# Performance work log

Measured on AMD Instinct MI355X. Metric: run time of the kernel, lower is better.

## Reference

```python
import jax, jax.numpy as jnp
import numpy as np

D_IN = 1024
D_OUT = 1024
NUM_HEADS = 16
HEAD_DIM = D_OUT // NUM_HEADS


def setup_inputs() -> dict:
    key = jax.random.key(0)
    ks = jax.random.split(key, 6)
    b, T = 2, 2048
    scale = 0.02
    x = jax.random.normal(ks[0], (b, T, D_IN), dtype=jnp.float32)
    Wq = jax.random.normal(ks[1], (D_IN, D_OUT), dtype=jnp.float32) * scale
    Wk = jax.random.normal(ks[2], (D_IN, D_OUT), dtype=jnp.float32) * scale
    Wv = jax.random.normal(ks[3], (D_IN, D_OUT), dtype=jnp.float32) * scale
    Wo = jax.random.normal(ks[4], (D_OUT, D_OUT), dtype=jnp.float32) * scale
    bo = jnp.zeros((D_OUT,), dtype=jnp.float32)
    return {"x": x, "Wq": Wq, "Wk": Wk, "Wv": Wv, "Wo": Wo, "bo": bo}


def reference(x, Wq, Wk, Wv, Wo, bo):
    b, T, _ = x.shape
    H, Dh = NUM_HEADS, HEAD_DIM
    # projections: [b,T,d_out] -> [b,H,T,Dh]
    q = (x @ Wq).reshape(b, T, H, Dh).transpose(0, 2, 1, 3)
    k = (x @ Wk).reshape(b, T, H, Dh).transpose(0, 2, 1, 3)
    v = (x @ Wv).reshape(b, T, H, Dh).transpose(0, 2, 1, 3)
    # scores: [b,H,T,T]
    att = jnp.einsum('bhqd,bhkd->bhqk', q, k)
    causal = jnp.triu(jnp.ones((T, T), dtype=bool), k=1)
    att = jnp.where(causal, -jnp.inf, att)
    att = jax.nn.softmax(att / np.sqrt(Dh).astype(np.float32), axis=-1)
    # dropout p=0.0 -> identity
    y = jnp.einsum('bhqk,bhkd->bhqd', att, v)
    y = y.transpose(0, 2, 1, 3).reshape(b, T, H * Dh)
    return y @ Wo + bo
```

## Files before the change

### kernel.cpp

```cpp
#include <hip/hip_runtime.h>

#define T_   2048
#define DM   1024
#define H_   16
#define DH   64

typedef unsigned short u16;
typedef unsigned int u32;
typedef __attribute__((ext_vector_type(8))) short bf16x8;
typedef __attribute__((ext_vector_type(8))) unsigned short u16x8;
typedef __attribute__((ext_vector_type(4))) float f32x4;
typedef __attribute__((ext_vector_type(16))) float f32x16;
typedef __attribute__((ext_vector_type(4))) unsigned int u32x4;
typedef __attribute__((ext_vector_type(2))) unsigned int u32x2;

static __device__ __forceinline__ u16 f2b(float f) {
  unsigned int u = __builtin_bit_cast(unsigned int, f);
  u += 0x7fff + ((u >> 16) & 1);
  return (u16)(u >> 16);
}

static __device__ __forceinline__ u32 cvtpk(float a, float b) {
  u32 d;
  asm("v_cvt_pk_bf16_f32 %0, %1, %2" : "=v"(d) : "v"(a), "v"(b));
  return d;
}

static __device__ __forceinline__ void gll16(const void* g, void* l) {
  __builtin_amdgcn_global_load_lds(
      (const __attribute__((address_space(1))) unsigned int*)g,
      (__attribute__((address_space(3))) unsigned int*)l, 16, 0, 0);
}

static __device__ __forceinline__ bf16x8 ldf(const char* base, int rho,
                                             int k16) {
  return *(const bf16x8*)(base + rho * 128 + ((k16 ^ (rho & 7)) << 4));
}


__global__ __launch_bounds__(256) void k_cvt_x(const float* __restrict__ x,
                                               u16* __restrict__ o) {
  int i = (blockIdx.x * 256 + threadIdx.x) * 8;
  float4 a = *(const float4*)(x + i);
  float4 b = *(const float4*)(x + i + 4);
  u16x8 r;
  r[0] = f2b(a.x); r[1] = f2b(a.y); r[2] = f2b(a.z); r[3] = f2b(a.w);
  r[4] = f2b(b.x); r[5] = f2b(b.y); r[6] = f2b(b.z); r[7] = f2b(b.w);
  *(u16x8*)(o + i) = r;
}

__global__ __launch_bounds__(256) void k_cvt_wt(
    const float* __restrict__ Wq, const float* __restrict__ Wk,
    const float* __restrict__ Wv, const float* __restrict__ Wo,
    u16* __restrict__ oq, u16* __restrict__ ok, u16* __restrict__ ov,
    u16* __restrict__ oo) {
  const float* W; u16* Wt;
  int z = blockIdx.z;
  if (z == 0)      { W = Wq; Wt = oq; }
  else if (z == 1) { W = Wk; Wt = ok; }
  else if (z == 2) { W = Wv; Wt = ov; }
  else             { W = Wo; Wt = oo; }
  const float wsc = (z == 0) ? 0.1803368801111204f : 1.0f;
  __shared__ u16 tile[64][65];
  int k0 = blockIdx.x * 64, n0 = blockIdx.y * 64;
  int r = threadIdx.x >> 2, c0 = (threadIdx.x & 3) * 16;
  const float* src = W + (k0 + r) * DM + n0 + c0;
#pragma unroll
  for (int e = 0; e < 16; e += 4) {
    float4 v = *(const float4*)(src + e);
    tile[r][c0 + e + 0] = f2b(v.x * wsc);
    tile[r][c0 + e + 1] = f2b(v.y * wsc);
    tile[r][c0 + e + 2] = f2b(v.z * wsc);
    tile[r][c0 + e + 3] = f2b(v.w * wsc);
  }
  __syncthreads();
  u16x8 a, b;
#pragma unroll
  for (int e = 0; e < 8; ++e) a[e] = tile[c0 + e][r];
#pragma unroll
  for (int e = 0; e < 8; ++e) b[e] = tile[c0 + 8 + e][r];
  u16* dst = Wt + (n0 + r) * DM + k0 + c0;
  *(u16x8*)dst = a;
  *(u16x8*)(dst + 8) = b;
}

__global__ __launch_bounds__(256) void k_qkv(
    const u16* __restrict__ X, const u16* __restrict__ Wqt,
    const u16* __restrict__ Wkt, const u16* __restrict__ Wvt,
    u16* __restrict__ Qg, u16* __restrict__ Kg, u16* __restrict__ Vtg) {
  __shared__ char smem[34816];
  char* As = smem;
  char* Bs = smem + 16384;
  const int tid = threadIdx.x, lane = tid & 63, w = tid >> 6;
  const int frow = lane & 15, fk = lane >> 4;
  const int wr = (w >> 1) * 64, wc = (w & 1) * 64;
  const int m0 = blockIdx.x * 128;
  const int by = blockIdx.y;
  const int z = by >> 3, n0 = (by & 7) * 128;
  const u16* Wt = (z == 0) ? Wqt : (z == 1) ? Wkt : Wvt;
  const u16* Ap = X + m0 * DM;
  const u16* Bp = Wt + n0 * DM;
  const int ro = lane >> 3;
  const int ce = ((lane & 7) ^ ro) << 3;

  f32x4 acc[4][4];
#pragma unroll
  for (int mi = 0; mi < 4; ++mi)
#pragma unroll
    for (int ni = 0; ni < 4; ++ni) acc[mi][ni] = (f32x4){0.f, 0.f, 0.f, 0.f};

  for (int k0 = 0; k0 < DM; k0 += 64) {
#pragma unroll
    for (int c = 0; c < 4; ++c) {
      const int g8 = (w * 4 + c) * 8;
      gll16(Ap + (g8 + ro) * DM + k0 + ce, As + g8 * 128);
      gll16(Bp + (g8 + ro) * DM + k0 + ce, Bs + g8 * 128);
    }
    asm volatile("s_waitcnt vmcnt(0)" ::: "memory");
    __syncthreads();
    bf16x8 a[4][2], b[4][2];
#pragma unroll
    for (int mi = 0; mi < 4; ++mi)
#pragma unroll
      for (int kk = 0; kk < 2; ++kk)
        a[mi][kk] = ldf(As, wr + mi * 16 + frow, kk * 4 + fk);
#pragma unroll
    for (int ni = 0; ni < 4; ++ni)
#pragma unroll
      for (int kk = 0; kk < 2; ++kk)
        b[ni][kk] = ldf(Bs, wc + ni * 16 + frow, kk * 4 + fk);
#pragma unroll
    for (int mi = 0; mi < 4; ++mi)
#pragma unroll
      for (int ni = 0; ni < 4; ++ni)
#pragma unroll
        for (int kk = 0; kk < 2; ++kk)
          acc[mi][ni] = __builtin_amdgcn_mfma_f32_16x16x32_bf16(
              a[mi][kk], b[ni][kk], acc[mi][ni], 0, 0, 0);
    __syncthreads();
  }

  if (z < 2) {
    u16* out = (z == 0) ? Qg : Kg;
#pragma unroll
    for (int mi = 0; mi < 4; ++mi)
#pragma unroll
      for (int ni = 0; ni < 4; ++ni)
#pragma unroll
        for (int r = 0; r < 4; ++r) {
          int m = m0 + wr + mi * 16 + fk * 4 + r;
          int nl = n0 + wc + ni * 16 + frow;
          int b = m >> 11, t = m & 2047, h = nl >> 6, d = nl & 63;
          out[((b * H_ + h) * T_ + t) * DH + d] = f2b(acc[mi][ni][r]);
        }
  } else {
    u16* Tl = (u16*)smem;
#pragma unroll
    for (int ni = 0; ni < 4; ++ni) {
      const int n = wc + ni * 16 + frow;
#pragma unroll
      for (int mi = 0; mi < 4; ++mi)
#pragma unroll
        for (int r = 0; r < 4; ++r)
          Tl[n * 136 + wr + mi * 16 + fk * 4 + r] = f2b(acc[mi][ni][r]);
    }
    __syncthreads();
    const int n = tid >> 1, c0 = (tid & 1) * 64;
    const int ng = n0 + n, h = ng >> 6, d = ng & 63;
    const int b = m0 >> 11;
    const int tb = (m0 & 2047) + c0;
    u16* dst = Vtg + ((b * H_ + h) * DH + d) * T_ + tb;
#pragma unroll
    for (int e = 0; e < 8; ++e)
      *(u16x8*)(dst + e * 8) = *(const u16x8*)(Tl + n * 136 + c0 + e * 8);
  }
}

__global__ __launch_bounds__(256) void k_out(
    const u16* __restrict__ Y, const u16* __restrict__ Wot,
    const float* __restrict__ bo, float* __restrict__ out) {
  __shared__ char smem[24576];
  char* As = smem;
  char* Bs = smem + 8192;
  const int tid = threadIdx.x, lane = tid & 63, w = tid >> 6;
  const int frow = lane & 15, fk = lane >> 4;
  const int wr = (w >> 1) * 32, wc = (w & 1) * 64;
  const int m0 = blockIdx.x * 64, n0 = blockIdx.y * 128;
  const u16* Ap = Y + m0 * DM;
  const u16* Bp = Wot + n0 * DM;
  const int ro = lane >> 3;
  const int ce = ((lane & 7) ^ ro) << 3;

  f32x4 acc[2][4];
#pragma unroll
  for (int mi = 0; mi < 2; ++mi)
#pragma unroll
    for (int ni = 0; ni < 4; ++ni) acc[mi][ni] = (f32x4){0.f, 0.f, 0.f, 0.f};

  for (int k0 = 0; k0 < DM; k0 += 64) {
#pragma unroll
    for (int c = 0; c < 2; ++c) {
      const int g8 = (w * 2 + c) * 8;
      gll16(Ap + (g8 + ro) * DM + k0 + ce, As + g8 * 128);
    }
#pragma unroll
    for (int c = 0; c < 4; ++c) {
      const int g8 = (w * 4 + c) * 8;
      gll16(Bp + (g8 + ro) * DM + k0 + ce, Bs + g8 * 128);
    }
    asm volatile("s_waitcnt vmcnt(0)" ::: "memory");
    __syncthreads();
    bf16x8 a[2][2], b[4][2];
#pragma unroll
    for (int mi = 0; mi < 2; ++mi)
#pragma unroll
      for (int kk = 0; kk < 2; ++kk)
        a[mi][kk] = ldf(As, wr + mi * 16 + frow, kk * 4 + fk);
#pragma unroll
    for (int ni = 0; ni < 4; ++ni)
#pragma unroll
      for (int kk = 0; kk < 2; ++kk)
        b[ni][kk] = ldf(Bs, wc + ni * 16 + frow, kk * 4 + fk);
#pragma unroll
    for (int mi = 0; mi < 2; ++mi)
#pragma unroll
      for (int ni = 0; ni < 4; ++ni)
#pragma unroll
        for (int kk = 0; kk < 2; ++kk)
          acc[mi][ni] = __builtin_amdgcn_mfma_f32_16x16x32_bf16(
              a[mi][kk], b[ni][kk], acc[mi][ni], 0, 0, 0);
    __syncthreads();
  }
#pragma unroll
  for (int mi = 0; mi < 2; ++mi)
#pragma unroll
    for (int ni = 0; ni < 4; ++ni)
#pragma unroll
      for (int r = 0; r < 4; ++r) {
        int m = m0 + wr + mi * 16 + fk * 4 + r;
        int n = n0 + wc + ni * 16 + frow;
        out[m * DM + n] = acc[mi][ni][r] + bo[n];
      }
}

__global__ __launch_bounds__(64) void k_attn(
    const u16* __restrict__ Qg, const u16* __restrict__ Kg,
    const u16* __restrict__ Vtg, u16* __restrict__ Yg) {
  __shared__ char Kl[8192];
  __shared__ char Vl[8192];
  const int bh = blockIdx.x;
  const int qt = 63 - blockIdx.y;
  const int q0 = qt * 32;
  const int lane = threadIdx.x;
  const int hi = lane >> 5, qq = lane & 31;
  const u16* Qb = Qg + bh * (T_ * DH);
  const u16* Kb = Kg + bh * (T_ * DH);
  const u16* Vb = Vtg + bh * (DH * T_);
  const int qrow = q0 + qq;

  bf16x8 qf[4];
#pragma unroll
  for (int kb = 0; kb < 4; ++kb)
    qf[kb] = *(const bf16x8*)(Qb + qrow * DH + kb * 16 + hi * 8);

  f32x16 o0, o1;
#pragma unroll
  for (int r = 0; r < 16; ++r) { o0[r] = 0.f; o1[r] = 0.f; }
  float m = -1e30f, lp = 0.f;

  const int nt = (qt >> 1) + 1;
  const int ro = lane >> 3;
  const int ce = ((lane & 7) ^ ro) << 3;

#pragma unroll
  for (int g = 0; g < 8; ++g)
    gll16(Kb + (g * 8 + ro) * DH + ce, Kl + g * 1024);
#pragma unroll
  for (int g = 0; g < 8; ++g)
    gll16(Vb + (g * 8 + ro) * T_ + ce, Vl + g * 1024);

  for (int t = 0; t < nt; ++t) {
    const bool st = (t + 1 < nt);
    const int jn = (t + 1) * 64;
    asm volatile("s_waitcnt vmcnt(8)" ::: "memory");
    bf16x8 kf[8];
#pragma unroll
    for (int kb = 0; kb < 4; ++kb) {
      kf[kb] = *(const bf16x8*)(
          Kl + qq * 128 + (((kb * 2 + hi) ^ (qq & 7)) << 4));
      kf[4 + kb] = *(const bf16x8*)(
          Kl + (qq + 32) * 128 + (((kb * 2 + hi) ^ (qq & 7)) << 4));
    }
    asm volatile("s_waitcnt lgkmcnt(0)" ::: "memory");
    if (st) {
#pragma unroll
      for (int g = 0; g < 8; ++g)
        gll16(Kb + (jn + g * 8 + ro) * DH + ce, Kl + g * 1024);
    }
    f32x16 s0, s1;
#pragma unroll
    for (int r = 0; r < 16; ++r) { s0[r] = 0.f; s1[r] = 0.f; }
#pragma unroll
    for (int kb = 0; kb < 4; ++kb) {
      s0 = __builtin_amdgcn_mfma_f32_32x32x16_bf16(kf[kb], qf[kb], s0, 0, 0, 0);
      s1 = __builtin_amdgcn_mfma_f32_32x32x16_bf16(kf[4 + kb], qf[kb], s1, 0, 0, 0);
    }
    if (t == nt - 1) {
      const int j0 = t * 64;
#pragma unroll
      for (int r = 0; r < 16; ++r) {
        const int cr = j0 + (r & 3) + 8 * (r >> 2) + 4 * hi;
        if (cr > qrow) s0[r] = -1e30f;
        if (cr + 32 > qrow) s1[r] = -1e30f;
      }
    }
    float tm[16];
#pragma unroll
    for (int r = 0; r < 16; ++r) tm[r] = fmaxf(s0[r], s1[r]);
#pragma unroll
    for (int stp = 8; stp > 0; stp >>= 1)
#pragma unroll
      for (int r = 0; r < stp; ++r) tm[r] = fmaxf(tm[r], tm[r + stp]);
    const float mt = fmaxf(tm[0], __shfl_xor(tm[0], 32));
    if (__any(mt > m + 8.f)) {
      const float mn = fmaxf(m, mt);
      const float al = __builtin_amdgcn_exp2f(m - mn);
      m = mn;
#pragma unroll
      for (int r = 0; r < 16; ++r) { o0[r] *= al; o1[r] *= al; }
      lp *= al;
    }
    float ts[16];
#pragma unroll
    for (int r = 0; r < 16; ++r) {
      s0[r] = __builtin_amdgcn_exp2f(s0[r] - m);
      s1[r] = __builtin_amdgcn_exp2f(s1[r] - m);
      ts[r] = s0[r] + s1[r];
    }
#pragma unroll
    for (int stp = 8; stp > 0; stp >>= 1)
#pragma unroll
      for (int r = 0; r < stp; ++r) ts[r] += ts[r + stp];
    lp += ts[0];
    bf16x8 pb[4];
#define MKCH(DST, S, RB)                                                     \
  {                                                                          \
    u32 a01 = cvtpk(S[RB + 0], S[RB + 1]);                                   \
    u32 a23 = cvtpk(S[RB + 2], S[RB + 3]);                                   \
    u32 a45 = cvtpk(S[RB + 4], S[RB + 5]);                                   \
    u32 a67 = cvtpk(S[RB + 6], S[RB + 7]);                                   \
    asm volatile("v_permlane32_swap_b32 %0, %1" : "+v"(a01), "+v"(a45));     \
    asm volatile("v_permlane32_swap_b32 %0, %1" : "+v"(a23), "+v"(a67));     \
    u32x4 t4;                                                                \
    t4[0] = a01; t4[1] = a23; t4[2] = a45; t4[3] = a67;                      \
    DST = __builtin_bit_cast(bf16x8, t4);                                    \
  }
    MKCH(pb[0], s0, 0)
    MKCH(pb[1], s0, 8)
    MKCH(pb[2], s1, 0)
    MKCH(pb[3], s1, 8)
#undef MKCH
    if (st) { asm volatile("s_waitcnt vmcnt(8)" ::: "memory"); }
    else    { asm volatile("s_waitcnt vmcnt(0)" ::: "memory"); }
    bf16x8 vf[8];
#pragma unroll
    for (int jc = 0; jc < 4; ++jc) {
      vf[jc] = *(const bf16x8*)(
          Vl + qq * 128 + (((jc * 2 + hi) ^ (qq & 7)) << 4));
      vf[4 + jc] = *(const bf16x8*)(
          Vl + (qq + 32) * 128 + (((jc * 2 + hi) ^ (qq & 7)) << 4));
    }
    asm volatile("s_waitcnt lgkmcnt(0)" ::: "memory");
    if (st) {
#pragma unroll
      for (int g = 0; g < 8; ++g)
        gll16(Vb + (g * 8 + ro) * T_ + jn + ce, Vl + g * 1024);
    }
#pragma unroll
    for (int jc = 0; jc < 4; ++jc) {
      o0 = __builtin_amdgcn_mfma_f32_32x32x16_bf16(vf[jc], pb[jc], o0, 0, 0, 0);
      o1 = __builtin_amdgcn_mfma_f32_32x32x16_bf16(vf[4 + jc], pb[jc], o1, 0, 0, 0);
    }
  }
  lp += __shfl_xor(lp, 32);
  const float rl = 1.0f / lp;
  const int obase = ((bh >> 4) * T_ + qrow) * DM + (bh & 15) * DH;
#pragma unroll
  for (int g = 0; g < 4; ++g) {
    u32x2 st;
    st[0] = cvtpk(o0[g * 4 + 0] * rl, o0[g * 4 + 1] * rl);
    st[1] = cvtpk(o0[g * 4 + 2] * rl, o0[g * 4 + 3] * rl);
    *(u32x2*)(Yg + obase + g * 8 + hi * 4) = st;
    st[0] = cvtpk(o1[g * 4 + 0] * rl, o1[g * 4 + 1] * rl);
    st[1] = cvtpk(o1[g * 4 + 2] * rl, o1[g * 4 + 3] * rl);
    *(u32x2*)(Yg + obase + 32 + g * 8 + hi * 4) = st;
  }
}


extern "C" void kernel_launch(void* const* d_in, const int* in_sizes, int n_in,
                              void* d_out, int out_size, void* d_ws,
                              size_t ws_size, hipStream_t stream) {
  const float* x  = (const float*)d_in[0];
  const float* Wq = (const float*)d_in[1];
  const float* Wk = (const float*)d_in[2];
  const float* Wv = (const float*)d_in[3];
  const float* Wo = (const float*)d_in[4];
  const float* bo = (const float*)d_in[5];
  float* out = (float*)d_out;
  char* ws = (char*)d_ws;

  u16* xb  = (u16*)(ws);
  u16* wqt = (u16*)(ws + (8ull << 20));
  u16* wkt = (u16*)(ws + (10ull << 20));
  u16* wvt = (u16*)(ws + (12ull << 20));
  u16* wot = (u16*)(ws + (14ull << 20));
  u16* Qg  = (u16*)(ws + (16ull << 20));
  u16* Kg  = (u16*)(ws + (24ull << 20));
  u16* Vtg = (u16*)(ws + (32ull << 20));
  u16* Yg  = (u16*)(ws + (40ull << 20));

  k_cvt_x<<<2048, 256, 0, stream>>>(x, xb);
  k_cvt_wt<<<dim3(16, 16, 4), 256, 0, stream>>>(Wq, Wk, Wv, Wo, wqt, wkt, wvt, wot);
  k_qkv<<<dim3(32, 24), 256, 0, stream>>>(xb, wqt, wkt, wvt, Qg, Kg, Vtg);
  k_attn<<<dim3(32, 64), 64, 0, stream>>>(Qg, Kg, Vtg, Yg);
  k_out<<<dim3(64, 8), 256, 0, stream>>>(Yg, wot, bo, out);
}
```

Baseline: 117.1 us.

## Double-buffer K/V LDS tiles in attention and raise MFMA wave priority

The attention kernel now keeps two LDS buffers each for K and V. It issues the next tile's global-to-LDS loads before reading the current tile, so the lgkmcnt waits that guarded single-buffer reuse are gone and the loads overlap with the LDS reads and MFMAs. s_setprio is raised around the MFMA blocks to favour matrix issue across waves. The cost is that LDS per block doubles to 32KB for a 64-thread block, which can cut how many blocks fit on a CU.

New measurement: 132.0 us. 1.13x slower.

```diff
diff --git a/kernel.cpp b/kernel.cpp
--- a/kernel.cpp
+++ b/kernel.cpp
@@ -11,7 +11,6 @@
 typedef __attribute__((ext_vector_type(8))) unsigned short u16x8;
 typedef __attribute__((ext_vector_type(4))) float f32x4;
 typedef __attribute__((ext_vector_type(16))) float f32x16;
-typedef __attribute__((ext_vector_type(4))) unsigned int u32x4;
 typedef __attribute__((ext_vector_type(2))) unsigned int u32x2;
 
 static __device__ __forceinline__ u16 f2b(float f) {
@@ -246,8 +245,8 @@
 __global__ __launch_bounds__(64) void k_attn(
     const u16* __restrict__ Qg, const u16* __restrict__ Kg,
     const u16* __restrict__ Vtg, u16* __restrict__ Yg) {
-  __shared__ char Kl[8192];
-  __shared__ char Vl[8192];
+  __shared__ char Kl[2][8192];
+  __shared__ char Vl[2][8192];
   const int bh = blockIdx.x;
   const int qt = 63 - blockIdx.y;
   const int q0 = qt * 32;
@@ -274,37 +273,42 @@
 
 #pragma unroll
   for (int g = 0; g < 8; ++g)
-    gll16(Kb + (g * 8 + ro) * DH + ce, Kl + g * 1024);
+    gll16(Kb + (g * 8 + ro) * DH + ce, Kl[0] + g * 1024);
 #pragma unroll
   for (int g = 0; g < 8; ++g)
-    gll16(Vb + (g * 8 + ro) * T_ + ce, Vl + g * 1024);
+    gll16(Vb + (g * 8 + ro) * T_ + ce, Vl[0] + g * 1024);
 
   for (int t = 0; t < nt; ++t) {
     const bool st = (t + 1 < nt);
     const int jn = (t + 1) * 64;
+    const char* Kc = Kl[t & 1];
+    const char* Vc = Vl[t & 1];
+    char* Kn = Kl[(t + 1) & 1];
+    char* Vn = Vl[(t + 1) & 1];
     asm volatile("s_waitcnt vmcnt(8)" ::: "memory");
+    if (st) {
+#pragma unroll
+      for (int g = 0; g < 8; ++g)
+        gll16(Kb + (jn + g * 8 + ro) * DH + ce, Kn + g * 1024);
+    }
     bf16x8 kf[8];
 #pragma unroll
     for (int kb = 0; kb < 4; ++kb) {
       kf[kb] = *(const bf16x8*)(
-          Kl + qq * 128 + (((kb * 2 + hi) ^ (qq & 7)) << 4));
+          Kc + qq * 128 + (((kb * 2 + hi) ^ (qq & 7)) << 4));
       kf[4 + kb] = *(const bf16x8*)(
-          Kl + (qq + 32) * 128 + (((kb * 2 + hi) ^ (qq & 7)) << 4));
-    }
-    asm volatile("s_waitcnt lgkmcnt(0)" ::: "memory");
-    if (st) {
-#pragma unroll
-      for (int g = 0; g < 8; ++g)
-        gll16(Kb + (jn + g * 8 + ro) * DH + ce, Kl + g * 1024);
+          Kc + (qq + 32) * 128 + (((kb * 2 + hi) ^ (qq & 7)) << 4));
     }
     f32x16 s0, s1;
 #pragma unroll
     for (int r = 0; r < 16; ++r) { s0[r] = 0.f; s1[r] = 0.f; }
+    __builtin_amdgcn_s_setprio(1);
 #pragma unroll
     for (int kb = 0; kb < 4; ++kb) {
       s0 = __builtin_amdgcn_mfma_f32_32x32x16_bf16(kf[kb], qf[kb], s0, 0, 0, 0);
       s1 = __builtin_amdgcn_mfma_f32_32x32x16_bf16(kf[4 + kb], qf[kb], s1, 0, 0, 0);
     }
+    __builtin_amdgcn_s_setprio(0);
     if (t == nt - 1) {
       const int j0 = t * 64;
 #pragma unroll
@@ -351,10 +355,11 @@
     u32 a67 = cvtpk(S[RB + 6], S[RB + 7]);                                   \
     asm volatile("v_permlane32_swap_b32 %0, %1" : "+v"(a01), "+v"(a45));     \
     asm volatile("v_permlane32_swap_b32 %0, %1" : "+v"(a23), "+v"(a67));     \
-    u32x4 t4;                                                                \
+    u32x4_t t4;                                                              \
     t4[0] = a01; t4[1] = a23; t4[2] = a45; t4[3] = a67;                      \
     DST = __builtin_bit_cast(bf16x8, t4);                                    \
   }
+    typedef __attribute__((ext_vector_type(4))) unsigned int u32x4_t;
     MKCH(pb[0], s0, 0)
     MKCH(pb[1], s0, 8)
     MKCH(pb[2], s1, 0)
@@ -362,25 +367,26 @@
 #undef MKCH
     if (st) { asm volatile("s_waitcnt vmcnt(8)" ::: "memory"); }
     else    { asm volatile("s_waitcnt vmcnt(0)" ::: "memory"); }
+    if (st) {
+#pragma unroll
+      for (int g = 0; g < 8; ++g)
+        gll16(Vb + (g * 8 + ro) * T_ + jn + ce, Vn + g * 1024);
+    }
     bf16x8 vf[8];
 #pragma unroll
     for (int jc = 0; jc < 4; ++jc) {
       vf[jc] = *(const bf16x8*)(
-          Vl + qq * 128 + (((jc * 2 + hi) ^ (qq & 7)) << 4));
+          Vc + qq * 128 + (((jc * 2 + hi) ^ (qq & 7)) << 4));
       vf[4 + jc] = *(const bf16x8*)(
-          Vl + (qq + 32) * 128 + (((jc * 2 + hi) ^ (qq & 7)) << 4));
-    }
-    asm volatile("s_waitcnt lgkmcnt(0)" ::: "memory");
-    if (st) {
-#pragma unroll
-      for (int g = 0; g < 8; ++g)
-        gll16(Vb + (g * 8 + ro) * T_ + jn + ce, Vl + g * 1024);
-    }
+          Vc + (qq + 32) * 128 + (((jc * 2 + hi) ^ (qq & 7)) << 4));
+    }
+    __builtin_amdgcn_s_setprio(1);
 #pragma unroll
     for (int jc = 0; jc < 4; ++jc) {
       o0 = __builtin_amdgcn_mfma_f32_32x32x16_bf16(vf[jc], pb[jc], o0, 0, 0, 0);
       o1 = __builtin_amdgcn_mfma_f32_32x32x16_bf16(vf[4 + jc], pb[jc], o1, 0, 0, 0);
     }
+    __builtin_amdgcn_s_setprio(0);
   }
   lp += __shfl_xor(lp, 32);
   const float rl = 1.0f / lp;
```
